# Kernel tuning notes

Hardware: AMD Instinct MI355X
Metric: run time of the kernel (lower is better)

Reference implementation:

```python
import jax, jax.numpy as jnp
import numpy as np

B, D_IN, D, C = 64, 1024, 768, 1000
EPS = 0.1        # args.alpha_cap
NUM_SIM = 3      # args.num_sim


def setup_inputs() -> dict:
    key = jax.random.key(0)
    k0, k1, k2, k3 = jax.random.split(key, 4)
    return {
        "x": jax.random.normal(k0, (B, D_IN), jnp.float32),
        "W_emb": jax.random.normal(k1, (D, D_IN), jnp.float32) * 0.02,
        "b_emb": jnp.zeros((D,), jnp.float32),
        "W_fc": jax.random.normal(k2, (C, D), jnp.float32) * 0.02,
        "b_fc": jnp.zeros((C,), jnp.float32),
        "anchors": jax.random.normal(k3, (C, D), jnp.float32),
    }


def _forward_core(x, W_emb, b_emb, W_fc, b_fc, anchors):
    # self.embedding(x): feature extractor -> [B, D]
    emb = x @ W_emb.T + b_emb
    # self.model(x) head logits -> [B, C]
    logits = emb @ W_fc.T + b_fc
    # compute_ulb_grads: grad of CE(fc(emb), onehot_j) wrt emb = (softmax - onehot_j) @ W_fc.
    # softmax is shared across all pseudo-labels j, so grad_ij = G_i - W_fc[j].
    p = jax.nn.softmax(logits, axis=-1)          # [B, C]
    G = p @ W_fc                                  # [B, D]
    grads = G[:, None, :] - W_fc[None, :, :]      # [B, C, D]
    # calculate_optimum_alpha: z = anchor - ulb_embed
    z = anchors[None, :, :] - emb[:, None, :]     # [B, C, D]
    z_norm = jnp.linalg.norm(z, axis=-1, keepdims=True)        # [B, C, 1]
    g_norm = jnp.linalg.norm(grads, axis=-1, keepdims=True)    # [B, C, 1]
    alpha = (EPS * z_norm / g_norm) * grads / (z + 1e-8)       # [B, C, D]
    # mix_feature: (1-alpha)*ulb_embed + alpha*anchor
    mix = (1.0 - alpha) * emb[:, None, :] + alpha * anchors[None, :, :]  # [B, C, D]
    # fc(feature_mix) -> [B, C, C]
    logits_mix = jnp.einsum('bjd,cd->bjc', mix, W_fc) + b_fc
    return logits, logits_mix


def reference(x, W_emb, b_emb, W_fc, b_fc, anchors):
    logits, logits_mix = _forward_core(x, W_emb, b_emb, W_fc, b_fc, anchors)
    predictions = jnp.argmax(logits, axis=-1)       # [B]
    preds_mix = jnp.argmax(logits_mix, axis=-1)     # [B, C]
    counts = jnp.zeros((B, C), jnp.float32)
    counts = counts.at[jnp.arange(B), predictions].add(1.0)
    counts = counts.at[jnp.arange(B)[:, None], preds_mix].add(1.0)
    # all_below_threshold: labels_count < num_sample everywhere
    return jnp.all(counts < NUM_SIM, axis=1)
```

## Files before the change

kernel.cpp:

```cpp
#include <hip/hip_runtime.h>
#include <stdint.h>
#include <stddef.h>

#define BB 64
#define DIN 1024
#define DD 768
#define CC 1000
#define EPSA 0.1f
#define NSIM 3

typedef short  s16x8 __attribute__((ext_vector_type(8)));
typedef float  f32x4 __attribute__((ext_vector_type(4)));

static __device__ __forceinline__ unsigned short f2bf_rne(float x) {
  unsigned u = __float_as_uint(x);
  return (unsigned short)((u + 0x7FFFu + ((u >> 16) & 1u)) >> 16);
}
static __device__ __forceinline__ float bf2f(unsigned short h) {
  return __uint_as_float(((unsigned)h) << 16);
}

__global__ __launch_bounds__(256) void prep_kernel(const float* __restrict__ W_fc,
                                                   const float* __restrict__ anchors,
                                                   const float* __restrict__ W_emb,
                                                   const float* __restrict__ x,
                                                   short* __restrict__ Bp, short* __restrict__ Ap,
                                                   short* __restrict__ Ip, short* __restrict__ Xp,
                                                   float* __restrict__ An2) {
  const int blk = blockIdx.x, tid = threadIdx.x;
  if (blk < 1184) {
    const float* src; short* dst; int KS, nrow, gid;
    if (blk < 384)       { src = W_fc;    dst = Bp; KS = 24; nrow = CC;  gid = blk * 256 + tid; }
    else if (blk < 768)  { src = anchors; dst = Ap; KS = 24; nrow = CC;  gid = (blk - 384) * 256 + tid; }
    else if (blk < 1152) { src = W_emb;   dst = Ip; KS = 32; nrow = DD;  gid = (blk - 768) * 256 + tid; }
    else                 { src = x;       dst = Xp; KS = 32; nrow = BB;  gid = (blk - 1152) * 256 + tid; }
    int lane = gid & 63;
    int ks   = (gid >> 6) % KS;
    int nt   = gid / (64 * KS);
    int row  = nt * 16 + (lane & 15);
    int k0   = ks * 32 + (lane >> 4) * 8;
    int stride = KS * 32;
    s16x8 v;
    #pragma unroll
    for (int r = 0; r < 8; ++r) {
      float w = (row < nrow) ? src[(size_t)row * stride + k0 + r] : 0.0f;
      v[r] = (short)f2bf_rne(w);
    }
    ((s16x8*)dst)[gid] = v;
  } else {
    int w = tid >> 6, lane = tid & 63;
    int j = (blk - 1184) * 4 + w;
    const float4* ar = (const float4*)(anchors + (size_t)j * DD);
    float an = 0.f;
    for (int k4 = lane; k4 < DD / 4; k4 += 64) {
      float4 a = ar[k4];
      an += a.x*a.x + a.y*a.y + a.z*a.z + a.w*a.w;
    }
    #pragma unroll
    for (int o = 1; o < 64; o <<= 1) an += __shfl_xor(an, o);
    if (lane == 0) An2[j] = an;
  }
}

__global__ __launch_bounds__(256) void embV_kernel(const short* __restrict__ Bp,
                                                   const short* __restrict__ Ip,
                                                   const short* __restrict__ Xp,
                                                   const float* __restrict__ b_emb,
                                                   unsigned short* __restrict__ Vb,
                                                   short* __restrict__ Vp,
                                                   float* __restrict__ emb,
                                                   short* __restrict__ Ep) {
  const int tid = threadIdx.x, w = tid >> 6, lane = tid & 63;
  __shared__ __attribute__((aligned(16))) short lsh[4608];
  if (blockIdx.x < 256) {
    const int bx = blockIdx.x & 15, cb = blockIdx.x >> 4;
    const int rnt = bx * 4 + w;
    const s16x8* BH = (const s16x8*)Bp;
    f32x4 acc[4] = {};
    for (int ks = 0; ks < 24; ++ks) {
      s16x8 a = BH[(rnt * 24 + ks) * 64 + lane];
      #pragma unroll
      for (int nf = 0; nf < 4; ++nf)
        acc[nf] = __builtin_amdgcn_mfma_f32_16x16x32_bf16(a, BH[((cb * 4 + nf) * 24 + ks) * 64 + lane], acc[nf], 0, 0, 0);
    }
    const int rl0 = (lane >> 4) * 4;
    const int r0 = rnt * 16 + rl0;
    const int c0 = cb * 64 + (lane & 15);
    #pragma unroll
    for (int nf = 0; nf < 4; ++nf)
      #pragma unroll
      for (int rr = 0; rr < 4; ++rr) {
        unsigned short h = f2bf_rne(acc[nf][rr]);
        Vb[(size_t)(r0 + rr) * 1024 + c0 + nf * 16] = h;
        lsh[w * 1152 + (rl0 + rr) * 72 + (lane & 15) + nf * 16] = (short)h;
      }
    __syncthreads();
    #pragma unroll
    for (int ksh = 0; ksh < 2; ++ksh) {
      int ks = cb * 2 + ksh;
      s16x8 v = *(const s16x8*)&lsh[w * 1152 + (lane & 15) * 72 + ksh * 32 + (lane >> 4) * 8];
      ((s16x8*)Vp)[(rnt * 32 + ks) * 64 + lane] = v;
    }
  } else {
    const int g = blockIdx.x - 256;
    const int nfr = g * 4 + w;
    const s16x8* XH = (const s16x8*)Xp;
    const s16x8* IH = (const s16x8*)Ip;
    f32x4 acc[4] = {};
    for (int ks = 0; ks < 32; ++ks) {
      s16x8 b = IH[(nfr * 32 + ks) * 64 + lane];
      #pragma unroll
      for (int mt = 0; mt < 4; ++mt)
        acc[mt] = __builtin_amdgcn_mfma_f32_16x16x32_bf16(XH[(mt * 32 + ks) * 64 + lane], b, acc[mt], 0, 0, 0);
    }
    const int d = nfr * 16 + (lane & 15);
    const int dl = w * 16 + (lane & 15);
    const float be = b_emb[d];
    #pragma unroll
    for (int mt = 0; mt < 4; ++mt)
      #pragma unroll
      for (int rr = 0; rr < 4; ++rr) {
        int b = mt * 16 + (lane >> 4) * 4 + rr;
        float ev = acc[mt][rr] + be;
        emb[(size_t)b * DD + d] = ev;
        lsh[b * 72 + dl] = (short)f2bf_rne(ev);
      }
    __syncthreads();
    #pragma unroll
    for (int ksh = 0; ksh < 2; ++ksh) {
      int ks = g * 2 + ksh;
      int mt2 = tid >> 6;
      s16x8 v = *(const s16x8*)&lsh[(mt2 * 16 + (lane & 15)) * 72 + ksh * 32 + (lane >> 4) * 8];
      ((s16x8*)Ep)[(mt2 * 24 + ks) * 64 + lane] = v;
    }
  }
}

__global__ __launch_bounds__(64) void logitsAE_kernel(const short* __restrict__ Ep,
                                                      const short* __restrict__ Bp,
                                                      const short* __restrict__ Ap,
                                                      const float* __restrict__ b_fc,
                                                      float* __restrict__ logits,
                                                      float* __restrict__ AE) {
  const int nfr = blockIdx.x;
  const int mt  = blockIdx.y;
  const int lane = threadIdx.x;
  const s16x8* E = (const s16x8*)Ep;
  const s16x8* B = (const s16x8*)Bp;
  const s16x8* A = (const s16x8*)Ap;
  f32x4 accL = {}, accA = {};
  for (int ks = 0; ks < 24; ++ks) {
    s16x8 a  = E[(mt * 24 + ks) * 64 + lane];
    s16x8 bW = B[(nfr * 24 + ks) * 64 + lane];
    s16x8 bA = A[(nfr * 24 + ks) * 64 + lane];
    accL = __builtin_amdgcn_mfma_f32_16x16x32_bf16(a, bW, accL, 0, 0, 0);
    accA = __builtin_amdgcn_mfma_f32_16x16x32_bf16(a, bA, accA, 0, 0, 0);
  }
  const int c = nfr * 16 + (lane & 15);
  if (c < CC) {
    const float bf = b_fc[c];
    #pragma unroll
    for (int rr = 0; rr < 4; ++rr) {
      int b = mt * 16 + (lane >> 4) * 4 + rr;
      logits[b * CC + c] = accL[rr] + bf;
      AE[b * CC + c]     = accA[rr];
    }
  }
}

__global__ __launch_bounds__(256) void softmax_kernel(const float* __restrict__ logits,
                                                      const float* __restrict__ emb,
                                                      float* __restrict__ p,
                                                      short* __restrict__ Pp,
                                                      int* __restrict__ pred,
                                                      float* __restrict__ En2) {
  const int b = blockIdx.x, t = threadIdx.x;
  const int w = t >> 6, lane = t & 63;
  __shared__ float ex[CC];
  __shared__ float sm[4]; __shared__ int si[4]; __shared__ float ss[4];
  __shared__ float sM, sS;

  float pe = 0.f;
  for (int k = t; k < DD; k += 256) { float e = emb[b * DD + k]; pe += e * e; }
  float m = -3.402823466e38f; int mi = 0;
  float lv[4];
  #pragma unroll
  for (int i = 0; i < 4; ++i) {
    int c = t + i * 256;
    float v = (c < CC) ? logits[b * CC + c] : -3.402823466e38f;
    lv[i] = v;
    if (v > m) { m = v; mi = c; }
  }
  #pragma unroll
  for (int o = 1; o < 64; o <<= 1) {
    float ov = __shfl_xor(m, o); int oi = __shfl_xor(mi, o);
    if (ov > m || (ov == m && oi < mi)) { m = ov; mi = oi; }
    pe += __shfl_xor(pe, o);
  }
  if (lane == 0) { sm[w] = m; si[w] = mi; ss[w] = pe; }
  __syncthreads();
  if (t == 0) {
    float M = sm[0]; int Mi = si[0];
    #pragma unroll
    for (int ww = 1; ww < 4; ++ww)
      if (sm[ww] > M || (sm[ww] == M && si[ww] < Mi)) { M = sm[ww]; Mi = si[ww]; }
    sM = M; pred[b] = Mi;
    En2[b] = ss[0] + ss[1] + ss[2] + ss[3];
  }
  __syncthreads();
  const float M = sM;
  float sum = 0.f;
  #pragma unroll
  for (int i = 0; i < 4; ++i) {
    int c = t + i * 256;
    if (c < CC) { float e = expf(lv[i] - M); ex[c] = e; sum += e; }
  }
  #pragma unroll
  for (int o = 1; o < 64; o <<= 1) sum += __shfl_xor(sum, o);
  if (lane == 0) ss[w] = sum;
  __syncthreads();
  if (t == 0) sS = ss[0] + ss[1] + ss[2] + ss[3];
  __syncthreads();
  const float S = sS;
  const int mt = b >> 4, blo = b & 15;
  for (int j = t; j < CC; j += 256) {
    float pj = ex[j] / S;
    p[b * CC + j] = pj;
    size_t fi = ((size_t)(mt * 32 + (j >> 5)) * 64 + ((j >> 3) & 3) * 16 + blo) * 8 + (j & 7);
    Pp[fi] = (short)f2bf_rne(pj);
  }
  if (t < 24) {
    int j = 1000 + t;
    size_t fi = ((size_t)(mt * 32 + (j >> 5)) * 64 + ((j >> 3) & 3) * 16 + blo) * 8 + (j & 7);
    Pp[fi] = 0;
  }
}

__global__ __launch_bounds__(64) void u_kernel(const short* __restrict__ Pp,
                                               const short* __restrict__ Vp,
                                               float* __restrict__ u) {
  const int nfr = blockIdx.x;
  const int mt  = blockIdx.y;
  const int lane = threadIdx.x;
  const s16x8* P = (const s16x8*)Pp;
  const s16x8* V = (const s16x8*)Vp;
  f32x4 acc = {};
  for (int ks = 0; ks < 32; ++ks) {
    s16x8 b = V[(nfr * 32 + ks) * 64 + lane];
    acc = __builtin_amdgcn_mfma_f32_16x16x32_bf16(P[(mt * 32 + ks) * 64 + lane], b, acc, 0, 0, 0);
  }
  const int c = nfr * 16 + (lane & 15);
  if (c < CC) {
    #pragma unroll
    for (int rr = 0; rr < 4; ++rr)
      u[(mt * 16 + (lane >> 4) * 4 + rr) * CC + c] = acc[rr];
  }
}

__global__ __launch_bounds__(256) void scan_kernel(const float* __restrict__ logits,
                                                   const float* __restrict__ u,
                                                   const float* __restrict__ p,
                                                   const float* __restrict__ AE,
                                                   const float* __restrict__ An2,
                                                   const float* __restrict__ En2,
                                                   const unsigned short* __restrict__ Vb,
                                                   unsigned long long* __restrict__ part) {
  const int b = blockIdx.x, cz = blockIdx.y;
  const int tid = threadIdx.x;
  const int c0 = cz * 63;
  const int cend = (CC - c0 < 63) ? (CC - c0) : 63;
  __shared__ __attribute__((aligned(8))) float2 LU[64];
  __shared__ float se[4];

  if (tid < cend) {
    int c = c0 + tid;
    LU[tid] = float2{logits[b * CC + c], u[b * CC + c]};
  }
  float partsum = 0.f;
  {
    int cg = tid * 4;
    if (cg + 3 < CC) {
      float4 p4 = *(const float4*)(p + b * CC + cg);
      float4 u4 = *(const float4*)(u + b * CC + cg);
      partsum = p4.x*u4.x + p4.y*u4.y + p4.z*u4.z + p4.w*u4.w;
    } else {
      #pragma unroll
      for (int i = 0; i < 4; ++i) {
        int c = cg + i;
        if (c < CC) partsum += p[b * CC + c] * u[b * CC + c];
      }
    }
  }
  #pragma unroll
  for (int o = 1; o < 64; o <<= 1) partsum += __shfl_xor(partsum, o);
  if ((tid & 63) == 0) se[tid >> 6] = partsum;
  __syncthreads();
  const float gn2b = se[0] + se[1] + se[2] + se[3];
  const float en2 = En2[b];

  const int jt = (tid < 250 ? tid : 249) * 4;
  float4 an4 = *(const float4*)(An2 + jt);
  float4 ae4 = *(const float4*)(AE + b * CC + jt);
  float4 uj4 = *(const float4*)(u + b * CC + jt);
  float sj[4], nsj[4];
  {
    float anv[4] = {an4.x, an4.y, an4.z, an4.w};
    float aev[4] = {ae4.x, ae4.y, ae4.z, ae4.w};
    float ujv[4] = {uj4.x, uj4.y, uj4.z, uj4.w};
    #pragma unroll
    for (int k = 0; k < 4; ++k) {
      float vd  = bf2f(Vb[(size_t)(jt + k) * 1024 + jt + k]);
      float zn2 = anv[k] - 2.0f * aev[k] + en2;
      float gn2 = gn2b - 2.0f * ujv[k] + vd;
      sj[k] = (EPSA * sqrtf(zn2)) / sqrtf(gn2);
      nsj[k] = -sj[k];
    }
  }

  float best[4] = {-3.402823466e38f, -3.402823466e38f, -3.402823466e38f, -3.402823466e38f};
  int   bi[4]   = {0, 0, 0, 0};
  const unsigned short* Vcol = Vb + jt;
  #pragma unroll 7
  for (int i = 0; i < cend; ++i) {
    int c = c0 + i;
    float2 lu = LU[i];
    uint2 vv = *(const uint2*)(Vcol + (size_t)c * 1024);
    float v0 = __uint_as_float(vv.x << 16);
    float v1 = __uint_as_float(vv.x & 0xffff0000u);
    float v2 = __uint_as_float(vv.y << 16);
    float v3 = __uint_as_float(vv.y & 0xffff0000u);
    float t0 = fmaf(sj[0], lu.y, lu.x);
    float t1 = fmaf(sj[1], lu.y, lu.x);
    float t2 = fmaf(sj[2], lu.y, lu.x);
    float t3 = fmaf(sj[3], lu.y, lu.x);
    float val0 = fmaf(nsj[0], v0, t0);
    float val1 = fmaf(nsj[1], v1, t1);
    float val2 = fmaf(nsj[2], v2, t2);
    float val3 = fmaf(nsj[3], v3, t3);
    if (val0 > best[0]) { best[0] = val0; bi[0] = c; }
    if (val1 > best[1]) { best[1] = val1; bi[1] = c; }
    if (val2 > best[2]) { best[2] = val2; bi[2] = c; }
    if (val3 > best[3]) { best[3] = val3; bi[3] = c; }
  }

  if (tid < 250) {
    unsigned long long* dst = part + ((size_t)(b * 1000 + jt)) * 16 + cz;
    #pragma unroll
    for (int k = 0; k < 4; ++k) {
      unsigned ub = __float_as_uint(best[k]);
      ub = (ub & 0x80000000u) ? ~ub : (ub | 0x80000000u);
      dst[(size_t)k * 16] = ((unsigned long long)ub << 32) |
                            (unsigned long long)(0xFFFFFFFFu - (unsigned)bi[k]);
    }
  }
}

__global__ __launch_bounds__(256) void counts_kernel(const unsigned long long* __restrict__ part,
                                                     const int* __restrict__ pred,
                                                     float* __restrict__ out) {
  int b = blockIdx.x, t = threadIdx.x;
  __shared__ int cnt[CC];
  __shared__ int bad;
  for (int c = t; c < CC; c += 256) cnt[c] = 0;
  if (t == 0) bad = 0;
  __syncthreads();
  if (t == 0) atomicAdd(&cnt[pred[b]], 1);
  for (int j = t; j < CC; j += 256) {
    const unsigned long long* q = part + ((size_t)(b * 1000 + j)) * 16;
    unsigned long long key = q[0];
    #pragma unroll
    for (int cz = 1; cz < 16; ++cz) {
      unsigned long long k2 = q[cz];
      key = (k2 > key) ? k2 : key;
    }
    int c = (int)(0xFFFFFFFFu - (unsigned)(key & 0xFFFFFFFFull));
    atomicAdd(&cnt[c], 1);
  }
  __syncthreads();
  for (int c = t; c < CC; c += 256) if (cnt[c] >= NSIM) bad = 1;
  __syncthreads();
  if (t == 0) out[b] = bad ? 0.0f : 1.0f;
}

extern "C" void kernel_launch(void* const* d_in, const int* in_sizes, int n_in,
                              void* d_out, int out_size, void* d_ws, size_t ws_size,
                              hipStream_t stream) {
  const float* x       = (const float*)d_in[0];
  const float* W_emb   = (const float*)d_in[1];
  const float* b_emb   = (const float*)d_in[2];
  const float* W_fc    = (const float*)d_in[3];
  const float* b_fc    = (const float*)d_in[4];
  const float* anchors = (const float*)d_in[5];
  float* out = (float*)d_out;

  float* emb    = (float*)d_ws;
  float* logits = emb + BB * DD;
  float* p      = logits + BB * CC;
  float* u      = p + BB * CC;
  float* AE     = u + BB * CC;
  float* An2    = AE + BB * CC;
  float* En2    = An2 + 1024;
  int*   pred   = (int*)(En2 + 64);
  unsigned long long* part = (unsigned long long*)(pred + 64);
  short* Bp     = (short*)(part + 64000 * 16);
  short* Ap     = Bp + 64 * 24 * 64 * 8;
  short* Ip     = Ap + 64 * 24 * 64 * 8;
  short* Xp     = Ip + 48 * 32 * 64 * 8;
  short* Ep     = Xp + 4 * 32 * 64 * 8;
  short* Pp     = Ep + 4 * 24 * 64 * 8;
  unsigned short* Vb = (unsigned short*)(Pp + 4 * 32 * 64 * 8);
  short* Vp     = (short*)(Vb + 1024 * 1024);

  hipLaunchKernelGGL(prep_kernel,    dim3(1434), dim3(256), 0, stream,
                     W_fc, anchors, W_emb, x, Bp, Ap, Ip, Xp, An2);
  hipLaunchKernelGGL(embV_kernel,    dim3(268), dim3(256), 0, stream,
                     Bp, Ip, Xp, b_emb, Vb, Vp, emb, Ep);
  hipLaunchKernelGGL(logitsAE_kernel,dim3(64, 4), dim3(64), 0, stream, Ep, Bp, Ap, b_fc, logits, AE);
  hipLaunchKernelGGL(softmax_kernel, dim3(BB), dim3(256), 0, stream, logits, emb, p, Pp, pred, En2);
  hipLaunchKernelGGL(u_kernel,       dim3(64, 4), dim3(64), 0, stream, Pp, Vp, u);
  hipLaunchKernelGGL(scan_kernel,    dim3(BB, 16), dim3(256), 0, stream,
                     logits, u, p, AE, An2, En2, Vb, part);
  hipLaunchKernelGGL(counts_kernel,  dim3(BB), dim3(256), 0, stream, part, pred, out);
}
```

Before: 74.37 us.

## Fuse logits, softmax and u GEMM into one kernel; halve scan split

Replaces the logitsAE, softmax and u kernels with a single lsu kernel per 16-row tile that keeps the logits tile and the bf16 probability fragments in shared memory. This removes two launches and the global round trip of logits and packed P. The scan kernel now processes 125 columns per block with 8 chunks instead of 16, halving partial-result storage and the counts reduction work. The fused kernel runs only 4 blocks, so the GEMM work is serialized across far fewer waves, and parallelism drops sharply.

Result: slower. 146.8 us (+97.4%).

```diff
diff --git a/kernel.cpp b/kernel.cpp
--- a/kernel.cpp
+++ b/kernel.cpp
@@ -8,6 +8,7 @@
 #define CC 1000
 #define EPSA 0.1f
 #define NSIM 3
+#define NEGINF -3.402823466e38f
 
 typedef short  s16x8 __attribute__((ext_vector_type(8)));
 typedef float  f32x4 __attribute__((ext_vector_type(4)));
@@ -136,124 +137,107 @@
   }
 }
 
-__global__ __launch_bounds__(64) void logitsAE_kernel(const short* __restrict__ Ep,
-                                                      const short* __restrict__ Bp,
-                                                      const short* __restrict__ Ap,
-                                                      const float* __restrict__ b_fc,
-                                                      float* __restrict__ logits,
-                                                      float* __restrict__ AE) {
-  const int nfr = blockIdx.x;
-  const int mt  = blockIdx.y;
-  const int lane = threadIdx.x;
+__global__ __launch_bounds__(512) void lsu_kernel(const short* __restrict__ Ep,
+                                                  const short* __restrict__ Bp,
+                                                  const short* __restrict__ Ap,
+                                                  const short* __restrict__ Vp,
+                                                  const float* __restrict__ b_fc,
+                                                  const float* __restrict__ emb,
+                                                  float* __restrict__ logits,
+                                                  float* __restrict__ AE,
+                                                  float* __restrict__ p,
+                                                  int* __restrict__ pred,
+                                                  float* __restrict__ En2,
+                                                  float* __restrict__ u) {
+  const int mt = blockIdx.x;
+  const int tid = threadIdx.x, w = tid >> 6, lane = tid & 63;
+  __shared__ __attribute__((aligned(16))) float Lt[16][1024];
+  __shared__ __attribute__((aligned(16))) short Pl[32 * 64 * 8];
   const s16x8* E = (const s16x8*)Ep;
   const s16x8* B = (const s16x8*)Bp;
   const s16x8* A = (const s16x8*)Ap;
-  f32x4 accL = {}, accA = {};
-  for (int ks = 0; ks < 24; ++ks) {
-    s16x8 a  = E[(mt * 24 + ks) * 64 + lane];
-    s16x8 bW = B[(nfr * 24 + ks) * 64 + lane];
-    s16x8 bA = A[(nfr * 24 + ks) * 64 + lane];
-    accL = __builtin_amdgcn_mfma_f32_16x16x32_bf16(a, bW, accL, 0, 0, 0);
-    accA = __builtin_amdgcn_mfma_f32_16x16x32_bf16(a, bA, accA, 0, 0, 0);
-  }
-  const int c = nfr * 16 + (lane & 15);
-  if (c < CC) {
-    const float bf = b_fc[c];
+
+  for (int nn = 0; nn < 8; ++nn) {
+    const int nfr = w + nn * 8;
+    f32x4 accL = {}, accA = {};
+    for (int ks = 0; ks < 24; ++ks) {
+      s16x8 a  = E[(mt * 24 + ks) * 64 + lane];
+      accL = __builtin_amdgcn_mfma_f32_16x16x32_bf16(a, B[(nfr * 24 + ks) * 64 + lane], accL, 0, 0, 0);
+      accA = __builtin_amdgcn_mfma_f32_16x16x32_bf16(a, A[(nfr * 24 + ks) * 64 + lane], accA, 0, 0, 0);
+    }
+    const int c = nfr * 16 + (lane & 15);
+    const float bf = (c < CC) ? b_fc[c] : 0.f;
     #pragma unroll
     for (int rr = 0; rr < 4; ++rr) {
-      int b = mt * 16 + (lane >> 4) * 4 + rr;
-      logits[b * CC + c] = accL[rr] + bf;
-      AE[b * CC + c]     = accA[rr];
-    }
-  }
-}
-
-__global__ __launch_bounds__(256) void softmax_kernel(const float* __restrict__ logits,
-                                                      const float* __restrict__ emb,
-                                                      float* __restrict__ p,
-                                                      short* __restrict__ Pp,
-                                                      int* __restrict__ pred,
-                                                      float* __restrict__ En2) {
-  const int b = blockIdx.x, t = threadIdx.x;
-  const int w = t >> 6, lane = t & 63;
-  __shared__ float ex[CC];
-  __shared__ float sm[4]; __shared__ int si[4]; __shared__ float ss[4];
-  __shared__ float sM, sS;
-
-  float pe = 0.f;
-  for (int k = t; k < DD; k += 256) { float e = emb[b * DD + k]; pe += e * e; }
-  float m = -3.402823466e38f; int mi = 0;
-  float lv[4];
-  #pragma unroll
-  for (int i = 0; i < 4; ++i) {
-    int c = t + i * 256;
-    float v = (c < CC) ? logits[b * CC + c] : -3.402823466e38f;
-    lv[i] = v;
-    if (v > m) { m = v; mi = c; }
-  }
-  #pragma unroll
-  for (int o = 1; o < 64; o <<= 1) {
-    float ov = __shfl_xor(m, o); int oi = __shfl_xor(mi, o);
-    if (ov > m || (ov == m && oi < mi)) { m = ov; mi = oi; }
-    pe += __shfl_xor(pe, o);
-  }
-  if (lane == 0) { sm[w] = m; si[w] = mi; ss[w] = pe; }
-  __syncthreads();
-  if (t == 0) {
-    float M = sm[0]; int Mi = si[0];
-    #pragma unroll
-    for (int ww = 1; ww < 4; ++ww)
-      if (sm[ww] > M || (sm[ww] == M && si[ww] < Mi)) { M = sm[ww]; Mi = si[ww]; }
-    sM = M; pred[b] = Mi;
-    En2[b] = ss[0] + ss[1] + ss[2] + ss[3];
-  }
-  __syncthreads();
-  const float M = sM;
-  float sum = 0.f;
-  #pragma unroll
-  for (int i = 0; i < 4; ++i) {
-    int c = t + i * 256;
-    if (c < CC) { float e = expf(lv[i] - M); ex[c] = e; sum += e; }
-  }
-  #pragma unroll
-  for (int o = 1; o < 64; o <<= 1) sum += __shfl_xor(sum, o);
-  if (lane == 0) ss[w] = sum;
-  __syncthreads();
-  if (t == 0) sS = ss[0] + ss[1] + ss[2] + ss[3];
-  __syncthreads();
-  const float S = sS;
-  const int mt = b >> 4, blo = b & 15;
-  for (int j = t; j < CC; j += 256) {
-    float pj = ex[j] / S;
-    p[b * CC + j] = pj;
-    size_t fi = ((size_t)(mt * 32 + (j >> 5)) * 64 + ((j >> 3) & 3) * 16 + blo) * 8 + (j & 7);
-    Pp[fi] = (short)f2bf_rne(pj);
-  }
-  if (t < 24) {
-    int j = 1000 + t;
-    size_t fi = ((size_t)(mt * 32 + (j >> 5)) * 64 + ((j >> 3) & 3) * 16 + blo) * 8 + (j & 7);
-    Pp[fi] = 0;
-  }
-}
-
-__global__ __launch_bounds__(64) void u_kernel(const short* __restrict__ Pp,
-                                               const short* __restrict__ Vp,
-                                               float* __restrict__ u) {
-  const int nfr = blockIdx.x;
-  const int mt  = blockIdx.y;
-  const int lane = threadIdx.x;
-  const s16x8* P = (const s16x8*)Pp;
+      int bl = (lane >> 4) * 4 + rr;
+      float lvv = accL[rr] + bf;
+      Lt[bl][c] = lvv;
+      if (c < CC) {
+        int b = mt * 16 + bl;
+        logits[b * CC + c] = lvv;
+        AE[b * CC + c]     = accA[rr];
+      }
+    }
+  }
+  __syncthreads();
+
+  for (int rep = 0; rep < 2; ++rep) {
+    const int blo = w + rep * 8;
+    const int b = mt * 16 + blo;
+    float pe = 0.f;
+    for (int k = lane; k < DD; k += 64) { float e = emb[b * DD + k]; pe += e * e; }
+    #pragma unroll
+    for (int o = 1; o < 64; o <<= 1) pe += __shfl_xor(pe, o);
+    if (lane == 0) En2[b] = pe;
+
+    float lv[16]; float m = NEGINF; int mi = 0;
+    #pragma unroll
+    for (int i = 0; i < 16; ++i) {
+      int c = lane + i * 64;
+      float v = (c < CC) ? Lt[blo][c] : NEGINF;
+      lv[i] = v;
+      if (v > m) { m = v; mi = c; }
+    }
+    #pragma unroll
+    for (int o = 1; o < 64; o <<= 1) {
+      float ov = __shfl_xor(m, o); int oi = __shfl_xor(mi, o);
+      if (ov > m || (ov == m && oi < mi)) { m = ov; mi = oi; }
+    }
+    if (lane == 0) pred[b] = mi;
+    float sum = 0.f;
+    #pragma unroll
+    for (int i = 0; i < 16; ++i) {
+      int c = lane + i * 64;
+      float e = (c < CC) ? expf(lv[i] - m) : 0.f;
+      lv[i] = e; sum += e;
+    }
+    #pragma unroll
+    for (int o = 1; o < 64; o <<= 1) sum += __shfl_xor(sum, o);
+    #pragma unroll
+    for (int i = 0; i < 16; ++i) {
+      int c = lane + i * 64;
+      float pj = lv[i] / sum;
+      unsigned short h = 0;
+      if (c < CC) { p[b * CC + c] = pj; h = f2bf_rne(pj); }
+      Pl[(((c >> 5) * 64) + ((c >> 3) & 3) * 16 + blo) * 8 + (c & 7)] = (short)h;
+    }
+  }
+  __syncthreads();
+
   const s16x8* V = (const s16x8*)Vp;
-  f32x4 acc = {};
-  for (int ks = 0; ks < 32; ++ks) {
-    s16x8 b = V[(nfr * 32 + ks) * 64 + lane];
-    acc = __builtin_amdgcn_mfma_f32_16x16x32_bf16(P[(mt * 32 + ks) * 64 + lane], b, acc, 0, 0, 0);
-  }
-  const int c = nfr * 16 + (lane & 15);
-  if (c < CC) {
-    #pragma unroll
-    for (int rr = 0; rr < 4; ++rr)
-      u[(mt * 16 + (lane >> 4) * 4 + rr) * CC + c] = acc[rr];
+  for (int nn = 0; nn < 8; ++nn) {
+    const int nfr = w + nn * 8;
+    f32x4 acc = {};
+    for (int ks = 0; ks < 32; ++ks) {
+      s16x8 a = *(const s16x8*)&Pl[(ks * 64 + lane) * 8];
+      acc = __builtin_amdgcn_mfma_f32_16x16x32_bf16(a, V[(nfr * 32 + ks) * 64 + lane], acc, 0, 0, 0);
+    }
+    const int c = nfr * 16 + (lane & 15);
+    if (c < CC) {
+      #pragma unroll
+      for (int rr = 0; rr < 4; ++rr)
+        u[(mt * 16 + (lane >> 4) * 4 + rr) * CC + c] = acc[rr];
+    }
   }
 }
 
@@ -267,12 +251,11 @@
                                                    unsigned long long* __restrict__ part) {
   const int b = blockIdx.x, cz = blockIdx.y;
   const int tid = threadIdx.x;
-  const int c0 = cz * 63;
-  const int cend = (CC - c0 < 63) ? (CC - c0) : 63;
-  __shared__ __attribute__((aligned(8))) float2 LU[64];
+  const int c0 = cz * 125;
+  __shared__ __attribute__((aligned(8))) float2 LU[128];
   __shared__ float se[4];
 
-  if (tid < cend) {
+  if (tid < 125) {
     int c = c0 + tid;
     LU[tid] = float2{logits[b * CC + c], u[b * CC + c]};
   }
@@ -317,11 +300,11 @@
     }
   }
 
-  float best[4] = {-3.402823466e38f, -3.402823466e38f, -3.402823466e38f, -3.402823466e38f};
+  float best[4] = {NEGINF, NEGINF, NEGINF, NEGINF};
   int   bi[4]   = {0, 0, 0, 0};
   const unsigned short* Vcol = Vb + jt;
-  #pragma unroll 7
-  for (int i = 0; i < cend; ++i) {
+  #pragma unroll 5
+  for (int i = 0; i < 125; ++i) {
     int c = c0 + i;
     float2 lu = LU[i];
     uint2 vv = *(const uint2*)(Vcol + (size_t)c * 1024);
@@ -344,13 +327,13 @@
   }
 
   if (tid < 250) {
-    unsigned long long* dst = part + ((size_t)(b * 1000 + jt)) * 16 + cz;
+    unsigned long long* dst = part + ((size_t)(b * 1000 + jt)) * 8 + cz;
     #pragma unroll
     for (int k = 0; k < 4; ++k) {
       unsigned ub = __float_as_uint(best[k]);
       ub = (ub & 0x80000000u) ? ~ub : (ub | 0x80000000u);
-      dst[(size_t)k * 16] = ((unsigned long long)ub << 32) |
-                            (unsigned long long)(0xFFFFFFFFu - (unsigned)bi[k]);
+      dst[(size_t)k * 8] = ((unsigned long long)ub << 32) |
+                           (unsigned long long)(0xFFFFFFFFu - (unsigned)bi[k]);
     }
   }
 }
@@ -366,10 +349,10 @@
   __syncthreads();
   if (t == 0) atomicAdd(&cnt[pred[b]], 1);
   for (int j = t; j < CC; j += 256) {
-    const unsigned long long* q = part + ((size_t)(b * 1000 + j)) * 16;
+    const unsigned long long* q = part + ((size_t)(b * 1000 + j)) * 8;
     unsigned long long key = q[0];
     #pragma unroll
-    for (int cz = 1; cz < 16; ++cz) {
+    for (int cz = 1; cz < 8; ++cz) {
       unsigned long long k2 = q[cz];
       key = (k2 > key) ? k2 : key;
     }
@@ -402,23 +385,21 @@
   float* En2    = An2 + 1024;
   int*   pred   = (int*)(En2 + 64);
   unsigned long long* part = (unsigned long long*)(pred + 64);
-  short* Bp     = (short*)(part + 64000 * 16);
+  short* Bp     = (short*)(part + 64000 * 8);
   short* Ap     = Bp + 64 * 24 * 64 * 8;
   short* Ip     = Ap + 64 * 24 * 64 * 8;
   short* Xp     = Ip + 48 * 32 * 64 * 8;
   short* Ep     = Xp + 4 * 32 * 64 * 8;
-  short* Pp     = Ep + 4 * 24 * 64 * 8;
-  unsigned short* Vb = (unsigned short*)(Pp + 4 * 32 * 64 * 8);
+  unsigned short* Vb = (unsigned short*)(Ep + 4 * 24 * 64 * 8);
   short* Vp     = (short*)(Vb + 1024 * 1024);
 
   hipLaunchKernelGGL(prep_kernel,    dim3(1434), dim3(256), 0, stream,
                      W_fc, anchors, W_emb, x, Bp, Ap, Ip, Xp, An2);
   hipLaunchKernelGGL(embV_kernel,    dim3(268), dim3(256), 0, stream,
                      Bp, Ip, Xp, b_emb, Vb, Vp, emb, Ep);
-  hipLaunchKernelGGL(logitsAE_kernel,dim3(64, 4), dim3(64), 0, stream, Ep, Bp, Ap, b_fc, logits, AE);
-  hipLaunchKernelGGL(softmax_kernel, dim3(BB), dim3(256), 0, stream, logits, emb, p, Pp, pred, En2);
-  hipLaunchKernelGGL(u_kernel,       dim3(64, 4), dim3(64), 0, stream, Pp, Vp, u);
-  hipLaunchKernelGGL(scan_kernel,    dim3(BB, 16), dim3(256), 0, stream,
+  hipLaunchKernelGGL(lsu_kernel,     dim3(4), dim3(512), 0, stream,
+                     Ep, Bp, Ap, Vp, b_fc, emb, logits, AE, p, pred, En2, u);
+  hipLaunchKernelGGL(scan_kernel,    dim3(BB, 8), dim3(256), 0, stream,
                      logits, u, p, AE, An2, En2, Vb, part);
   hipLaunchKernelGGL(counts_kernel,  dim3(BB), dim3(256), 0, stream, part, pred, out);
 }
```
